# Kernel optimization log

Hardware: AMD Instinct MI355X
Metric: run time of the kernel (lower is better)

Reference implementation:

```python
import jax, jax.numpy as jnp
import numpy as np

B, N, C, H = 8, 1025, 768, 12
HD = C // H  # 64
SCALE = HD ** -0.5


def rotate_half(x):
    x1, x2 = jnp.split(x, 2, axis=-1)
    return jnp.concatenate((-x2, x1), axis=-1)


def apply_rope(x, sin, cos):
    return x * cos + rotate_half(x) * sin


def setup_inputs() -> dict:
    key = jax.random.key(0)
    ks = jax.random.split(key, 7)
    x = jax.random.normal(ks[0], (B, N, C), dtype=jnp.float32)
    sin = jax.random.normal(ks[1], (N - 1, HD), dtype=jnp.float32)
    cos = jax.random.normal(ks[2], (N - 1, HD), dtype=jnp.float32)
    s = 1.0 / np.sqrt(C)
    qkv_w = jax.random.normal(ks[3], (3 * C, C), dtype=jnp.float32) * s
    qkv_b = jnp.zeros((3 * C,), dtype=jnp.float32)
    proj_w = jax.random.normal(ks[4], (C, C), dtype=jnp.float32) * s
    proj_b = jnp.zeros((C,), dtype=jnp.float32)
    return {"x": x, "sin": sin, "cos": cos, "qkv_w": qkv_w, "qkv_b": qkv_b,
            "proj_w": proj_w, "proj_b": proj_b}


def reference(x, sin, cos, qkv_w, qkv_b, proj_w, proj_b):
    b, n, c = x.shape
    qkv = x @ qkv_w.T + qkv_b                      # [B,N,3C]
    qkv = qkv.reshape(b, n, 3, H, HD)
    qkv = jnp.transpose(qkv, (2, 0, 3, 1, 4))      # [3,B,H,N,HD]
    q, k, v = qkv[0], qkv[1], qkv[2]
    # RoPE on patch tokens only (cls token at index 0 excluded)
    q_patch = apply_rope(q[:, :, 1:, :], sin, cos)
    k_patch = apply_rope(k[:, :, 1:, :], sin, cos)
    q = jnp.concatenate((q[:, :, :1, :], q_patch), axis=2)
    k = jnp.concatenate((k[:, :, :1, :], k_patch), axis=2)
    attn = jnp.einsum('bhqd,bhkd->bhqk', q, k) * SCALE
    attn = jax.nn.softmax(attn, axis=-1)
    out = jnp.einsum('bhqk,bhkd->bhqd', attn, v)   # [B,H,N,HD]
    out = jnp.transpose(out, (0, 2, 1, 3)).reshape(b, n, c)
    out = out @ proj_w.T + proj_b
    return out
```

## Files before the change

kernel.cpp:

```cpp
#include <hip/hip_runtime.h>
#include <hip/hip_bf16.h>

constexpr int NTOK   = 1025;
constexpr int M      = 8 * NTOK;
constexpr int MP     = 8448;
constexpr int KDIM   = 768;
constexpr int NQKV   = 2304;
constexpr int NKVPAD = 1088;
constexpr float SCALEL2 = 0.125f * 1.44269504f;

using bf16x8 = __attribute__((ext_vector_type(8))) short;
using f32x4  = __attribute__((ext_vector_type(4))) float;

__device__ __forceinline__ f32x4 mfma_bf16(bf16x8 a, bf16x8 b, f32x4 c) {
  return __builtin_amdgcn_mfma_f32_16x16x32_bf16(a, b, c, 0, 0, 0);
}

__device__ __forceinline__ void gl16(const void* g, void* l) {
  __builtin_amdgcn_global_load_lds(
      (const __attribute__((address_space(1))) void*)g,
      (__attribute__((address_space(3))) void*)l, 16, 0, 0);
}

template <int N> __device__ __forceinline__ void wait_vmcnt() {
  if constexpr (N == 0)
    asm volatile("s_waitcnt vmcnt(0)" ::: "memory");
  else if constexpr (N == 4)
    asm volatile("s_waitcnt vmcnt(4)" ::: "memory");
  else if constexpr (N == 6)
    asm volatile("s_waitcnt vmcnt(6)" ::: "memory");
}

__device__ __forceinline__ float exp2_raw(float x) {
  float r;
  asm("v_exp_f32 %0, %1" : "=v"(r) : "v"(x));
  return r;
}
__device__ __forceinline__ unsigned short cvt_bf16_u16(float x) {
  unsigned u;
  asm("v_cvt_pk_bf16_f32 %0, %1, %2" : "=v"(u) : "v"(x), "v"(x));
  return (unsigned short)(u & 0xffffu);
}
__device__ __forceinline__ __hip_bfloat16 cvt_bf16_raw(float x) {
  union { unsigned short s; __hip_bfloat16 b; } c;
  c.s = cvt_bf16_u16(x);
  return c.b;
}

constexpr size_t SZ_X     = (size_t)MP * KDIM * 2;
constexpr size_t SZ_WQ    = (size_t)NQKV * KDIM * 2;
constexpr size_t SZ_PW    = (size_t)KDIM * KDIM * 2;
constexpr size_t SZ_QK    = (size_t)96 * NTOK * 64 * 2;
constexpr size_t SZ_VT    = (size_t)96 * 64 * NKVPAD * 2;
constexpr size_t OFF_XHI  = 0;
constexpr size_t OFF_WQHI = OFF_XHI + SZ_X;
constexpr size_t OFF_PWHI = OFF_WQHI + SZ_WQ;
constexpr size_t OFF_PWLO = OFF_PWHI + SZ_PW;
constexpr size_t OFF_Q    = OFF_PWLO + SZ_PW;
constexpr size_t OFF_K    = OFF_Q + SZ_QK;
constexpr size_t OFF_VT   = OFF_K + SZ_QK;
constexpr size_t OFF_AO   = OFF_VT + SZ_VT;

constexpr int N4_X  = MP * KDIM / 4;
constexpr int N4_WQ = NQKV * KDIM / 4;
constexpr int N4_PW = KDIM * KDIM / 4;
constexpr int NPADC = NKVPAD - NTOK;
constexpr int N4_PAD = 96 * 64 * NPADC / 4;
constexpr int N4_TOT = N4_X + N4_WQ + N4_PW + N4_PAD;

__global__ void k_prep(const float* __restrict__ x, const float* __restrict__ qkvw,
                       const float* __restrict__ projw,
                       __hip_bfloat16* __restrict__ xhi,
                       __hip_bfloat16* __restrict__ wqhi,
                       __hip_bfloat16* __restrict__ pwhi,
                       __hip_bfloat16* __restrict__ pwlo,
                       __hip_bfloat16* __restrict__ vt) {
  const int u = blockIdx.x * 256 + threadIdx.x;
  if (u < N4_X) {
    const int i = u * 4;
    ushort4 o = {0, 0, 0, 0};
    if (i < M * KDIM) {
      const float4 v = *(const float4*)(x + i);
      o = ushort4{cvt_bf16_u16(v.x), cvt_bf16_u16(v.y), cvt_bf16_u16(v.z),
                  cvt_bf16_u16(v.w)};
    }
    *(ushort4*)((unsigned short*)xhi + i) = o;
  } else if (u < N4_X + N4_WQ) {
    const int i = (u - N4_X) * 4;
    const float4 v = *(const float4*)(qkvw + i);
    *(ushort4*)((unsigned short*)wqhi + i) = ushort4{
        cvt_bf16_u16(v.x), cvt_bf16_u16(v.y), cvt_bf16_u16(v.z), cvt_bf16_u16(v.w)};
  } else if (u < N4_X + N4_WQ + N4_PW) {
    const int i = (u - N4_X - N4_WQ) * 4;
    const float4 v = *(const float4*)(projw + i);
    float vv[4] = {v.x, v.y, v.z, v.w};
    unsigned short h[4], l[4];
#pragma unroll
    for (int k = 0; k < 4; ++k) {
      h[k] = cvt_bf16_u16(vv[k]);
      union { unsigned ui; float f; } c;
      c.ui = (unsigned)h[k] << 16;
      l[k] = cvt_bf16_u16(vv[k] - c.f);
    }
    *(ushort4*)((unsigned short*)pwhi + i) = ushort4{h[0], h[1], h[2], h[3]};
    *(ushort4*)((unsigned short*)pwlo + i) = ushort4{l[0], l[1], l[2], l[3]};
  } else {
    const int e0 = (u - N4_X - N4_WQ - N4_PW) * 4;
#pragma unroll
    for (int k = 0; k < 4; ++k) {
      const int e = e0 + k;
      const int r = e / NPADC;
      const int c = NTOK + (e - r * NPADC);
      vt[(size_t)r * NKVPAD + c] = __float2bfloat16(0.0f);
    }
  }
}

template <int NBX>
__global__ __launch_bounds__(512) void k_gemm_qkv(
    const __hip_bfloat16* __restrict__ A, const __hip_bfloat16* __restrict__ B,
    const float* __restrict__ bias, const float* __restrict__ sinp,
    const float* __restrict__ cosp, __hip_bfloat16* __restrict__ o_q,
    __hip_bfloat16* __restrict__ o_k, __hip_bfloat16* __restrict__ o_vt) {
  const int tid = threadIdx.x;
  const int w = tid >> 6, lane = tid & 63;
  const int wm = w >> 1, wn = w & 1;
  const int l15 = lane & 15, q4 = lane >> 4;

  const int nwg = gridDim.x;
  const int orig = blockIdx.x;
  const int qc = nwg >> 3, rc = nwg & 7;
  const int xcd = orig & 7, o8 = orig >> 3;
  const int wg =
      (xcd < rc ? xcd * (qc + 1) : rc * (qc + 1) + (xcd - rc) * qc) + o8;
  const int bx = wg % NBX, by = wg / NBX;
  const int mBase = by * 256, nBase = bx * 128;

  __shared__ __hip_bfloat16 sm[2][12288];
  constexpr int OFFB = 16384;

  const char* pA = (const char*)A + (size_t)mBase * 1536;
  const char* pB = (const char*)B + (size_t)nBase * 1536;

  int sA_src[2], sA_dst[2], sB_src, sB_dst;
#pragma unroll
  for (int i = 0; i < 2; ++i) {
    const int c = i * 512 + tid;
    const int row = c >> 2;
    sA_src[i] = row * 1536 + (((c & 3) ^ ((row >> 1) & 3)) << 4);
    sA_dst[i] = c << 4;
  }
  {
    const int c = tid;
    const int row = c >> 2;
    sB_src = row * 1536 + (((c & 3) ^ ((row >> 1) & 3)) << 4);
    sB_dst = c << 4;
  }
  auto stage = [&](int kt, int buf) {
    const int kofs = kt * 64;
    char* base = (char*)&sm[buf][0];
#pragma unroll
    for (int i = 0; i < 2; ++i) gl16(pA + sA_src[i] + kofs, base + sA_dst[i]);
    gl16(pB + sB_src + kofs, base + OFFB + sB_dst);
  };

  int fA[4], fB[4];
#pragma unroll
  for (int f = 0; f < 4; ++f) {
    const int ra = wm * 64 + f * 16 + l15;
    const int rb = wn * 64 + f * 16 + l15;
    fA[f] = ra * 64 + ((q4 ^ ((ra >> 1) & 3)) << 4);
    fB[f] = OFFB + rb * 64 + ((q4 ^ ((rb >> 1) & 3)) << 4);
  }

  f32x4 acc[4][4] = {};

  stage(0, 0);
  __syncthreads();

  constexpr int NKT = KDIM / 32;
  for (int kt = 0; kt < NKT; ++kt) {
    const int cur = kt & 1;
    if (kt + 1 < NKT) stage(kt + 1, cur ^ 1);
    const char* s = (const char*)&sm[cur][0];
    bf16x8 a[4], b[4];
#pragma unroll
    for (int f = 0; f < 4; ++f) {
      a[f] = *(const bf16x8*)(s + fA[f]);
      b[f] = *(const bf16x8*)(s + fB[f]);
    }
    __builtin_amdgcn_s_setprio(1);
#pragma unroll
    for (int mt = 0; mt < 4; ++mt)
#pragma unroll
      for (int nt = 0; nt < 4; ++nt)
        acc[mt][nt] = mfma_bf16(a[mt], b[nt], acc[mt][nt]);
    __builtin_amdgcn_s_setprio(0);
    __syncthreads();
  }

#pragma unroll
  for (int mt = 0; mt < 4; ++mt)
#pragma unroll
    for (int j = 0; j < 4; ++j) {
      const int gm = mBase + wm * 64 + mt * 16 + q4 * 4 + j;
      if (gm >= M) continue;
      const int b = gm / NTOK;
      const int t = gm - b * NTOK;
#pragma unroll
      for (int nt = 0; nt < 4; ++nt) {
        const int gc = nBase + wn * 64 + nt * 16 + l15;
        float v = acc[mt][nt][j] + bias[gc];
        const int three = gc / 768;
        const int hd = gc - three * 768;
        const int h = hd >> 6, d = hd & 63;
        const int bh = b * 12 + h;
        if (three == 2) {
          o_vt[((size_t)bh * 64 + d) * NKVPAD + t] = __float2bfloat16(v);
        } else {
          if (t > 0) {
            const float pv = acc[mt][nt ^ 2][j] + bias[gc ^ 32];
            const int so = (t - 1) * 64 + d;
            v = v * cosp[so] + ((d < 32) ? -pv : pv) * sinp[so];
          }
          if (three == 0)
            o_q[((size_t)bh * NTOK + t) * 64 + d] = __float2bfloat16(v);
          else
            o_k[((size_t)bh * NTOK + t) * 64 + d] = __float2bfloat16(v * SCALEL2);
        }
      }
    }
}

template <int NBX>
__global__ __launch_bounds__(256) void k_gemm_proj(
    const __hip_bfloat16* __restrict__ Ahi, const __hip_bfloat16* __restrict__ Asec,
    const __hip_bfloat16* __restrict__ Bhi, const float* __restrict__ bias,
    float* __restrict__ o_f32) {
  const int tid = threadIdx.x;
  const int w = tid >> 6, lane = tid & 63;
  const int wm = w >> 1, wn = w & 1;
  const int l15 = lane & 15, q4 = lane >> 4;

  const int nwg = gridDim.x;
  const int orig = blockIdx.x;
  const int qc = nwg >> 3, rc = nwg & 7;
  const int xcd = orig & 7, o8 = orig >> 3;
  const int wg =
      (xcd < rc ? xcd * (qc + 1) : rc * (qc + 1) + (xcd - rc) * qc) + o8;
  const int bx = wg % NBX, by = wg / NBX;
  const int mBase = by * 128, nBase = bx * 128;

  __shared__ __hip_bfloat16 sm[3][3 * 4096];

  const char* p0 = (const char*)Ahi + (size_t)mBase * (KDIM * 2);
  const char* p1 = (const char*)Asec + (size_t)nBase * (KDIM * 2);
  const char* p2 = (const char*)Bhi + (size_t)nBase * (KDIM * 2);

  const int slog = ((tid & 3) ^ ((tid >> 3) & 3)) << 4;
  const int ph = ((q4 ^ ((l15 >> 1) & 3)) << 4);

  auto stage = [&](int kt, int buf) {
    const int kofs = kt * 64;
    char* base = (char*)sm[buf];
#pragma unroll
    for (int i = 0; i < 2; ++i) {
      const int c = i * 256 + tid;
      const size_t rb = (size_t)(i * 64 + (tid >> 2)) * (KDIM * 2) + slog + kofs;
      gl16(p0 + rb, base + (size_t)c * 16);
      gl16(p1 + rb, base + 8192 + (size_t)c * 16);
      gl16(p2 + rb, base + 16384 + (size_t)c * 16);
    }
  };

  f32x4 acc[4][4] = {};

  stage(0, 0);
  stage(1, 1);

  constexpr int NKT = KDIM / 32;
  for (int kt = 0; kt < NKT; ++kt) {
    if (kt < NKT - 1)
      wait_vmcnt<6>();
    else
      wait_vmcnt<0>();
    __builtin_amdgcn_s_barrier();
    if (kt + 2 < NKT) stage(kt + 2, (kt + 2) % 3);
    char* s0 = (char*)sm[kt % 3];
    char* s1 = s0 + 8192;
    char* s2 = s0 + 16384;
    bf16x8 a0[4], b0[4], b1[4];
#pragma unroll
    for (int mt = 0; mt < 4; ++mt) {
      const int r = wm * 64 + mt * 16 + l15;
      a0[mt] = *(const bf16x8*)(s0 + r * 64 + ph);
    }
#pragma unroll
    for (int nt = 0; nt < 4; ++nt) {
      const int r = wn * 64 + nt * 16 + l15;
      b0[nt] = *(const bf16x8*)(s2 + r * 64 + ph);
      b1[nt] = *(const bf16x8*)(s1 + r * 64 + ph);
    }
    __builtin_amdgcn_s_setprio(1);
#pragma unroll
    for (int mt = 0; mt < 4; ++mt)
#pragma unroll
      for (int nt = 0; nt < 4; ++nt) {
        acc[mt][nt] = mfma_bf16(a0[mt], b0[nt], acc[mt][nt]);
        acc[mt][nt] = mfma_bf16(a0[mt], b1[nt], acc[mt][nt]);
      }
    __builtin_amdgcn_s_setprio(0);
  }

#pragma unroll
  for (int mt = 0; mt < 4; ++mt)
#pragma unroll
    for (int j = 0; j < 4; ++j) {
      const int gm = mBase + wm * 64 + mt * 16 + q4 * 4 + j;
      if (gm >= M) continue;
#pragma unroll
      for (int nt = 0; nt < 4; ++nt) {
        const int gc = nBase + wn * 64 + nt * 16 + l15;
        o_f32[(size_t)gm * 768 + gc] = acc[mt][nt][j] + bias[gc];
      }
    }
}

__global__ __launch_bounds__(256) void k_attn(
    const __hip_bfloat16* __restrict__ Q, const __hip_bfloat16* __restrict__ Kk,
    const __hip_bfloat16* __restrict__ VT, __hip_bfloat16* __restrict__ ao) {
  __shared__ __hip_bfloat16 Kt[3][64 * 64];
  __shared__ __hip_bfloat16 Vt[3][64 * 64];
  __shared__ __hip_bfloat16 Pl[4][32][72];
  const int tid = threadIdx.x, w = tid >> 6, lane = tid & 63;
  const int l15 = lane & 15, q4 = lane >> 4;
  const int id = blockIdx.x;
  const int xcd = id & 7, sub = id >> 3;
  const int hh = sub / 9;
  const int bh = xcd * 12 + hh;
  const int qb = (sub - hh * 9) * 128 + w * 32;
  const size_t qbase = (size_t)bh * NTOK * 64;
  const char* Kb = (const char*)(Kk + qbase);
  const char* Vb = (const char*)(VT + (size_t)bh * 64 * NKVPAD);

  int frag_off[2][4];
#pragma unroll
  for (int f = 0; f < 4; ++f) {
    const int row = f * 16 + l15;
#pragma unroll
    for (int ks = 0; ks < 2; ++ks)
      frag_off[ks][f] = row * 128 + (((ks * 4 + q4) ^ (row & 7)) << 4);
  }
  int stRow[2], sch16[2], stK[2], stV[2], ldsOff[2];
#pragma unroll
  for (int i = 0; i < 2; ++i) {
    const int c = i * 256 + tid;
    const int row = c >> 3;
    stRow[i] = row;
    sch16[i] = ((c & 7) ^ (row & 7)) << 4;
    stK[i] = row * 128 + sch16[i];
    stV[i] = row * (NKVPAD * 2) + sch16[i];
    ldsOff[i] = c * 16;
  }
  int pw_off[2][4], pa_off[2][2];
#pragma unroll
  for (int mt = 0; mt < 2; ++mt) {
#pragma unroll
    for (int j = 0; j < 4; ++j)
      pw_off[mt][j] = ((w * 32 + mt * 16 + q4 * 4 + j) * 72 + l15) * 2;
#pragma unroll
    for (int ks = 0; ks < 2; ++ks)
      pa_off[mt][ks] = ((w * 32 + mt * 16 + l15) * 72 + ks * 32 + q4 * 8) * 2;
  }
  char* Plc = (char*)&Pl[0][0][0];

  bf16x8 qa[2][2];
#pragma unroll
  for (int mt = 0; mt < 2; ++mt) {
    int t = qb + mt * 16 + l15;
    if (t > NTOK - 1) t = NTOK - 1;
#pragma unroll
    for (int ks = 0; ks < 2; ++ks)
      qa[mt][ks] = *(const bf16x8*)(Q + qbase + (size_t)t * 64 + ks * 32 + q4 * 8);
  }

  f32x4 accO[2][4] = {};
  float mrun[2][4], lpart[2][4];
#pragma unroll
  for (int mt = 0; mt < 2; ++mt)
#pragma unroll
    for (int j = 0; j < 4; ++j) {
      mrun[mt][j] = -1e30f;
      lpart[mt][j] = 0.0f;
    }

  auto stageKV = [&](int kt, int b) {
    const int kb0 = kt * 64;
#pragma unroll
    for (int i = 0; i < 2; ++i) {
      const char* srcK;
      if (kt == 16) {
        const int srow = min(kb0 + stRow[i], NTOK - 1);
        srcK = Kb + (size_t)srow * 128 + sch16[i];
      } else {
        srcK = Kb + (size_t)kb0 * 128 + stK[i];
      }
      gl16(srcK, (char*)&Kt[b][0] + ldsOff[i]);
      gl16(Vb + (size_t)kb0 * 2 + stV[i], (char*)&Vt[b][0] + ldsOff[i]);
    }
  };

  auto step = [&](int kt, int cur, bool last) {
    f32x4 s[2][4] = {};
    {
      const char* Kc = (const char*)&Kt[cur][0];
      bf16x8 kfr[2][4];
#pragma unroll
      for (int nt = 0; nt < 4; ++nt)
#pragma unroll
        for (int ks = 0; ks < 2; ++ks)
          kfr[ks][nt] = *(const bf16x8*)(Kc + frag_off[ks][nt]);
      __builtin_amdgcn_s_setprio(1);
#pragma unroll
      for (int mt = 0; mt < 2; ++mt)
#pragma unroll
        for (int nt = 0; nt < 4; ++nt)
#pragma unroll
          for (int ks = 0; ks < 2; ++ks)
            s[mt][nt] = mfma_bf16(qa[mt][ks], kfr[ks][nt], s[mt][nt]);
      __builtin_amdgcn_s_setprio(0);
    }
    if (last) {
#pragma unroll
      for (int nt = 0; nt < 4; ++nt)
        if (1024 + nt * 16 + l15 > NTOK - 1) {
#pragma unroll
          for (int mt = 0; mt < 2; ++mt)
#pragma unroll
            for (int j = 0; j < 4; ++j) s[mt][nt][j] = -1e30f;
        }
    }
    float smax[2][4];
    bool okl = true;
#pragma unroll
    for (int mt = 0; mt < 2; ++mt)
#pragma unroll
      for (int j = 0; j < 4; ++j) {
        const float a =
            fmaxf(fmaxf(s[mt][0][j], s[mt][1][j]), fmaxf(s[mt][2][j], s[mt][3][j]));
        smax[mt][j] = a;
        okl = okl && (a <= mrun[mt][j] + 8.0f);
      }
    if (!__all((int)okl)) {
#pragma unroll
      for (int mt = 0; mt < 2; ++mt)
#pragma unroll
        for (int j = 0; j < 4; ++j) {
          float m0 = smax[mt][j];
#pragma unroll
          for (int off = 1; off < 16; off <<= 1) m0 = fmaxf(m0, __shfl_xor(m0, off));
          const float mnew = fmaxf(mrun[mt][j], m0);
          const float fsc = exp2_raw(mrun[mt][j] - mnew);
          lpart[mt][j] *= fsc;
          mrun[mt][j] = mnew;
#pragma unroll
          for (int nd = 0; nd < 4; ++nd) accO[mt][nd][j] *= fsc;
        }
    }
#pragma unroll
    for (int mt = 0; mt < 2; ++mt)
#pragma unroll
      for (int j = 0; j < 4; ++j) {
        float acc = 0.0f;
        char* pw = Plc + pw_off[mt][j];
#pragma unroll
        for (int nt = 0; nt < 4; ++nt) {
          const float p = exp2_raw(s[mt][nt][j] - mrun[mt][j]);
          acc += p;
          *(__hip_bfloat16*)(pw + nt * 32) = cvt_bf16_raw(p);
        }
        lpart[mt][j] += acc;
      }
    bf16x8 pa[2][2], vf[2][4];
#pragma unroll
    for (int mt = 0; mt < 2; ++mt)
#pragma unroll
      for (int ks = 0; ks < 2; ++ks)
        pa[mt][ks] = *(const bf16x8*)(Plc + pa_off[mt][ks]);
    {
      const char* Vc = (const char*)&Vt[cur][0];
#pragma unroll
      for (int nd = 0; nd < 4; ++nd)
#pragma unroll
        for (int ks = 0; ks < 2; ++ks)
          vf[ks][nd] = *(const bf16x8*)(Vc + frag_off[ks][nd]);
    }
    __builtin_amdgcn_s_setprio(1);
#pragma unroll
    for (int mt = 0; mt < 2; ++mt)
#pragma unroll
      for (int nd = 0; nd < 4; ++nd)
#pragma unroll
        for (int ks = 0; ks < 2; ++ks)
          accO[mt][nd] = mfma_bf16(pa[mt][ks], vf[ks][nd], accO[mt][nd]);
    __builtin_amdgcn_s_setprio(0);
  };

  stageKV(0, 0);
  stageKV(1, 1);
  for (int kt = 0; kt < 17; ++kt) {
    if (kt < 16)
      wait_vmcnt<4>();
    else
      wait_vmcnt<0>();
    __builtin_amdgcn_s_barrier();
    if (kt + 2 < 17) stageKV(kt + 2, (kt + 2) % 3);
    step(kt, kt % 3, kt == 16);
  }

  const int b = bh / 12, h = bh - (bh / 12) * 12;
#pragma unroll
  for (int mt = 0; mt < 2; ++mt)
#pragma unroll
    for (int j = 0; j < 4; ++j) {
      float sum = lpart[mt][j];
#pragma unroll
      for (int off2 = 1; off2 < 16; off2 <<= 1) sum += __shfl_xor(sum, off2);
      const int t = qb + mt * 16 + q4 * 4 + j;
      if (t > NTOK - 1) continue;
      const float inv = 1.0f / sum;
      const size_t ro = ((size_t)(b * NTOK + t)) * 768 + h * 64;
#pragma unroll
      for (int nd = 0; nd < 4; ++nd) {
        const int d = nd * 16 + l15;
        ao[ro + d] = __float2bfloat16(accO[mt][nd][j] * inv);
      }
    }
}

extern "C" void kernel_launch(void* const* d_in, const int* in_sizes, int n_in,
                              void* d_out, int out_size, void* d_ws, size_t ws_size,
                              hipStream_t stream) {
  const float* x = (const float*)d_in[0];
  const float* sinp = (const float*)d_in[1];
  const float* cosp = (const float*)d_in[2];
  const float* qkvw = (const float*)d_in[3];
  const float* qkvb = (const float*)d_in[4];
  const float* projw = (const float*)d_in[5];
  const float* projb = (const float*)d_in[6];

  char* ws = (char*)d_ws;
  __hip_bfloat16* xhi = (__hip_bfloat16*)(ws + OFF_XHI);
  __hip_bfloat16* wqhi = (__hip_bfloat16*)(ws + OFF_WQHI);
  __hip_bfloat16* pwhi = (__hip_bfloat16*)(ws + OFF_PWHI);
  __hip_bfloat16* pwlo = (__hip_bfloat16*)(ws + OFF_PWLO);
  __hip_bfloat16* qb = (__hip_bfloat16*)(ws + OFF_Q);
  __hip_bfloat16* kb = (__hip_bfloat16*)(ws + OFF_K);
  __hip_bfloat16* vt = (__hip_bfloat16*)(ws + OFF_VT);
  __hip_bfloat16* ao = (__hip_bfloat16*)(ws + OFF_AO);

  k_prep<<<N4_TOT / 256, 256, 0, stream>>>(x, qkvw, projw, xhi, wqhi, pwhi, pwlo,
                                           vt);
  k_gemm_qkv<18><<<dim3(18 * 33), 512, 0, stream>>>(xhi, wqhi, qkvb, sinp, cosp,
                                                    qb, kb, vt);
  k_attn<<<dim3(864), 256, 0, stream>>>(qb, kb, vt, ao);
  k_gemm_proj<6><<<dim3(6 * 66), 256, 0, stream>>>(ao, pwlo, pwhi, projb,
                                                   (float*)d_out);
}
```

Before: 235.6 us.

## Retile QKV GEMM to 128x256 with 4 waves and triple-buffered LDS pipeline

The QKV projection GEMM moves from 256x128 tiles with 8 waves to 128x256 tiles with 4 waves, each wave computing a 64x128 sub-tile. LDS staging changes from double to triple buffering, using vmcnt waits and a raw barrier in place of __syncthreads, so global loads run two k-steps ahead. The padded M shrinks to 8320, which reduces the number of M tiles for both GEMMs. The aim is more MFMA work per LDS read and better overlap of loads with compute, at the cost of higher register pressure from 32 accumulators per wave and more LDS per block.

```diff
diff --git a/kernel.cpp b/kernel.cpp
--- a/kernel.cpp
+++ b/kernel.cpp
@@ -3,7 +3,7 @@
 
 constexpr int NTOK   = 1025;
 constexpr int M      = 8 * NTOK;
-constexpr int MP     = 8448;
+constexpr int MP     = 8320;
 constexpr int KDIM   = 768;
 constexpr int NQKV   = 2304;
 constexpr int NKVPAD = 1088;
@@ -117,7 +117,7 @@
 }
 
 template <int NBX>
-__global__ __launch_bounds__(512) void k_gemm_qkv(
+__global__ __launch_bounds__(256) void k_gemm_qkv(
     const __hip_bfloat16* __restrict__ A, const __hip_bfloat16* __restrict__ B,
     const float* __restrict__ bias, const float* __restrict__ sinp,
     const float* __restrict__ cosp, __hip_bfloat16* __restrict__ o_q,
@@ -134,69 +134,76 @@
   const int wg =
       (xcd < rc ? xcd * (qc + 1) : rc * (qc + 1) + (xcd - rc) * qc) + o8;
   const int bx = wg % NBX, by = wg / NBX;
-  const int mBase = by * 256, nBase = bx * 128;
-
-  __shared__ __hip_bfloat16 sm[2][12288];
-  constexpr int OFFB = 16384;
+  const int mBase = by * 128, nBase = bx * 256;
+
+  __shared__ __hip_bfloat16 sm[3][12288];
+  constexpr int OFFB = 8192;
 
   const char* pA = (const char*)A + (size_t)mBase * 1536;
   const char* pB = (const char*)B + (size_t)nBase * 1536;
 
-  int sA_src[2], sA_dst[2], sB_src, sB_dst;
+  int sA_src[2], sA_dst[2], sB_src[4], sB_dst[4];
 #pragma unroll
   for (int i = 0; i < 2; ++i) {
-    const int c = i * 512 + tid;
+    const int c = i * 256 + tid;
     const int row = c >> 2;
     sA_src[i] = row * 1536 + (((c & 3) ^ ((row >> 1) & 3)) << 4);
     sA_dst[i] = c << 4;
   }
-  {
-    const int c = tid;
+#pragma unroll
+  for (int i = 0; i < 4; ++i) {
+    const int c = i * 256 + tid;
     const int row = c >> 2;
-    sB_src = row * 1536 + (((c & 3) ^ ((row >> 1) & 3)) << 4);
-    sB_dst = c << 4;
+    sB_src[i] = row * 1536 + (((c & 3) ^ ((row >> 1) & 3)) << 4);
+    sB_dst[i] = OFFB + (c << 4);
   }
   auto stage = [&](int kt, int buf) {
     const int kofs = kt * 64;
     char* base = (char*)&sm[buf][0];
 #pragma unroll
     for (int i = 0; i < 2; ++i) gl16(pA + sA_src[i] + kofs, base + sA_dst[i]);
-    gl16(pB + sB_src + kofs, base + OFFB + sB_dst);
+#pragma unroll
+    for (int i = 0; i < 4; ++i) gl16(pB + sB_src[i] + kofs, base + sB_dst[i]);
   };
 
-  int fA[4], fB[4];
+  int fA[4], fB[8];
 #pragma unroll
   for (int f = 0; f < 4; ++f) {
     const int ra = wm * 64 + f * 16 + l15;
-    const int rb = wn * 64 + f * 16 + l15;
     fA[f] = ra * 64 + ((q4 ^ ((ra >> 1) & 3)) << 4);
+  }
+#pragma unroll
+  for (int f = 0; f < 8; ++f) {
+    const int rb = wn * 128 + f * 16 + l15;
     fB[f] = OFFB + rb * 64 + ((q4 ^ ((rb >> 1) & 3)) << 4);
   }
 
-  f32x4 acc[4][4] = {};
+  f32x4 acc[4][8] = {};
 
   stage(0, 0);
-  __syncthreads();
+  stage(1, 1);
 
   constexpr int NKT = KDIM / 32;
   for (int kt = 0; kt < NKT; ++kt) {
-    const int cur = kt & 1;
-    if (kt + 1 < NKT) stage(kt + 1, cur ^ 1);
-    const char* s = (const char*)&sm[cur][0];
-    bf16x8 a[4], b[4];
-#pragma unroll
-    for (int f = 0; f < 4; ++f) {
-      a[f] = *(const bf16x8*)(s + fA[f]);
-      b[f] = *(const bf16x8*)(s + fB[f]);
-    }
+    if (kt < NKT - 1)
+      wait_vmcnt<6>();
+    else
+      wait_vmcnt<0>();
+    __builtin_amdgcn_s_barrier();
+    if (kt + 2 < NKT) stage(kt + 2, (kt + 2) % 3);
+    const char* s = (const char*)&sm[kt % 3][0];
+    bf16x8 a[4], b[8];
+#pragma unroll
+    for (int f = 0; f < 4; ++f) a[f] = *(const bf16x8*)(s + fA[f]);
+#pragma unroll
+    for (int f = 0; f < 8; ++f) b[f] = *(const bf16x8*)(s + fB[f]);
     __builtin_amdgcn_s_setprio(1);
 #pragma unroll
     for (int mt = 0; mt < 4; ++mt)
 #pragma unroll
-      for (int nt = 0; nt < 4; ++nt)
+      for (int nt = 0; nt < 8; ++nt)
         acc[mt][nt] = mfma_bf16(a[mt], b[nt], acc[mt][nt]);
     __builtin_amdgcn_s_setprio(0);
-    __syncthreads();
   }
 
 #pragma unroll
@@ -208,8 +215,8 @@
       const int b = gm / NTOK;
       const int t = gm - b * NTOK;
 #pragma unroll
-      for (int nt = 0; nt < 4; ++nt) {
-        const int gc = nBase + wn * 64 + nt * 16 + l15;
+      for (int nt = 0; nt < 8; ++nt) {
+        const int gc = nBase + wn * 128 + nt * 16 + l15;
         float v = acc[mt][nt][j] + bias[gc];
         const int three = gc / 768;
         const int hd = gc - three * 768;
@@ -561,9 +568,9 @@
 
   k_prep<<<N4_TOT / 256, 256, 0, stream>>>(x, qkvw, projw, xhi, wqhi, pwhi, pwlo,
                                            vt);
-  k_gemm_qkv<18><<<dim3(18 * 33), 512, 0, stream>>>(xhi, wqhi, qkvb, sinp, cosp,
-                                                    qb, kb, vt);
+  k_gemm_qkv<9><<<dim3(9 * 65), 256, 0, stream>>>(xhi, wqhi, qkvb, sinp, cosp,
+                                                  qb, kb, vt);
   k_attn<<<dim3(864), 256, 0, stream>>>(qb, kb, vt, ao);
-  k_gemm_proj<6><<<dim3(6 * 66), 256, 0, stream>>>(ao, pwlo, pwhi, projb,
+  k_gemm_proj<6><<<dim3(6 * 65), 256, 0, stream>>>(ao, pwlo, pwhi, projb,
                                                    (float*)d_out);
 }
```

Result: slower. 293.7 us (+24.7%).

## Drop proj weight low split and enlarge QKV GEMM tile with triple buffering

Applied to the files above, without the earlier changes.

The projection GEMM no longer uses the hi/lo bf16 split of the weights. It now runs a single bf16 MFMA per tile, which halves its MFMA work and LDS traffic, and the prep kernel stops writing the low part. The QKV GEMM grows its tile from 256x128 to 256x256, with 8 waves arranged 2x4 and each wave covering a 128x64 slab. It also moves from a double-buffered __syncthreads pipeline to a three-stage global_load_lds pipeline using vmcnt waits. The larger tile and 48KB of LDS per buffer set give more reuse but fewer workgroups (297) and more accumulator registers, and dropping the low split reduces projection precision.

```diff
diff --git a/kernel.cpp b/kernel.cpp
--- a/kernel.cpp
+++ b/kernel.cpp
@@ -55,8 +55,7 @@
 constexpr size_t OFF_XHI  = 0;
 constexpr size_t OFF_WQHI = OFF_XHI + SZ_X;
 constexpr size_t OFF_PWHI = OFF_WQHI + SZ_WQ;
-constexpr size_t OFF_PWLO = OFF_PWHI + SZ_PW;
-constexpr size_t OFF_Q    = OFF_PWLO + SZ_PW;
+constexpr size_t OFF_Q    = OFF_PWHI + SZ_PW;
 constexpr size_t OFF_K    = OFF_Q + SZ_QK;
 constexpr size_t OFF_VT   = OFF_K + SZ_QK;
 constexpr size_t OFF_AO   = OFF_VT + SZ_VT;
@@ -73,7 +72,6 @@
                        __hip_bfloat16* __restrict__ xhi,
                        __hip_bfloat16* __restrict__ wqhi,
                        __hip_bfloat16* __restrict__ pwhi,
-                       __hip_bfloat16* __restrict__ pwlo,
                        __hip_bfloat16* __restrict__ vt) {
   const int u = blockIdx.x * 256 + threadIdx.x;
   if (u < N4_X) {
@@ -93,17 +91,8 @@
   } else if (u < N4_X + N4_WQ + N4_PW) {
     const int i = (u - N4_X - N4_WQ) * 4;
     const float4 v = *(const float4*)(projw + i);
-    float vv[4] = {v.x, v.y, v.z, v.w};
-    unsigned short h[4], l[4];
-#pragma unroll
-    for (int k = 0; k < 4; ++k) {
-      h[k] = cvt_bf16_u16(vv[k]);
-      union { unsigned ui; float f; } c;
-      c.ui = (unsigned)h[k] << 16;
-      l[k] = cvt_bf16_u16(vv[k] - c.f);
-    }
-    *(ushort4*)((unsigned short*)pwhi + i) = ushort4{h[0], h[1], h[2], h[3]};
-    *(ushort4*)((unsigned short*)pwlo + i) = ushort4{l[0], l[1], l[2], l[3]};
+    *(ushort4*)((unsigned short*)pwhi + i) = ushort4{
+        cvt_bf16_u16(v.x), cvt_bf16_u16(v.y), cvt_bf16_u16(v.z), cvt_bf16_u16(v.w)};
   } else {
     const int e0 = (u - N4_X - N4_WQ - N4_PW) * 4;
 #pragma unroll
@@ -124,7 +113,7 @@
     __hip_bfloat16* __restrict__ o_k, __hip_bfloat16* __restrict__ o_vt) {
   const int tid = threadIdx.x;
   const int w = tid >> 6, lane = tid & 63;
-  const int wm = w >> 1, wn = w & 1;
+  const int wm = w >> 2, wn = w & 3;
   const int l15 = lane & 15, q4 = lane >> 4;
 
   const int nwg = gridDim.x;
@@ -134,76 +123,77 @@
   const int wg =
       (xcd < rc ? xcd * (qc + 1) : rc * (qc + 1) + (xcd - rc) * qc) + o8;
   const int bx = wg % NBX, by = wg / NBX;
-  const int mBase = by * 256, nBase = bx * 128;
-
-  __shared__ __hip_bfloat16 sm[2][12288];
+  const int mBase = by * 256, nBase = bx * 256;
+
+  __shared__ __hip_bfloat16 sm[3][16384];
   constexpr int OFFB = 16384;
 
   const char* pA = (const char*)A + (size_t)mBase * 1536;
   const char* pB = (const char*)B + (size_t)nBase * 1536;
 
-  int sA_src[2], sA_dst[2], sB_src, sB_dst;
+  int sSrc[2], sDst[2];
 #pragma unroll
   for (int i = 0; i < 2; ++i) {
     const int c = i * 512 + tid;
     const int row = c >> 2;
-    sA_src[i] = row * 1536 + (((c & 3) ^ ((row >> 1) & 3)) << 4);
-    sA_dst[i] = c << 4;
-  }
-  {
-    const int c = tid;
-    const int row = c >> 2;
-    sB_src = row * 1536 + (((c & 3) ^ ((row >> 1) & 3)) << 4);
-    sB_dst = c << 4;
+    sSrc[i] = row * 1536 + (((c & 3) ^ ((row >> 1) & 3)) << 4);
+    sDst[i] = c << 4;
   }
   auto stage = [&](int kt, int buf) {
     const int kofs = kt * 64;
     char* base = (char*)&sm[buf][0];
 #pragma unroll
-    for (int i = 0; i < 2; ++i) gl16(pA + sA_src[i] + kofs, base + sA_dst[i]);
-    gl16(pB + sB_src + kofs, base + OFFB + sB_dst);
+    for (int i = 0; i < 2; ++i) {
+      gl16(pA + sSrc[i] + kofs, base + sDst[i]);
+      gl16(pB + sSrc[i] + kofs, base + OFFB + sDst[i]);
+    }
   };
 
-  int fA[4], fB[4];
+  int fA[8], fB[4];
+#pragma unroll
+  for (int f = 0; f < 8; ++f) {
+    const int ra = wm * 128 + f * 16 + l15;
+    fA[f] = ra * 64 + ((q4 ^ ((ra >> 1) & 3)) << 4);
+  }
 #pragma unroll
   for (int f = 0; f < 4; ++f) {
-    const int ra = wm * 64 + f * 16 + l15;
     const int rb = wn * 64 + f * 16 + l15;
-    fA[f] = ra * 64 + ((q4 ^ ((ra >> 1) & 3)) << 4);
     fB[f] = OFFB + rb * 64 + ((q4 ^ ((rb >> 1) & 3)) << 4);
   }
 
-  f32x4 acc[4][4] = {};
+  f32x4 acc[8][4] = {};
 
   stage(0, 0);
-  __syncthreads();
+  stage(1, 1);
 
   constexpr int NKT = KDIM / 32;
   for (int kt = 0; kt < NKT; ++kt) {
-    const int cur = kt & 1;
-    if (kt + 1 < NKT) stage(kt + 1, cur ^ 1);
-    const char* s = (const char*)&sm[cur][0];
-    bf16x8 a[4], b[4];
-#pragma unroll
-    for (int f = 0; f < 4; ++f) {
-      a[f] = *(const bf16x8*)(s + fA[f]);
-      b[f] = *(const bf16x8*)(s + fB[f]);
-    }
+    if (kt < NKT - 1)
+      wait_vmcnt<4>();
+    else
+      wait_vmcnt<0>();
+    __builtin_amdgcn_s_barrier();
+    if (kt + 2 < NKT) stage(kt + 2, (kt + 2) % 3);
+    const char* s = (const char*)&sm[kt % 3][0];
+    bf16x8 a[8], b[4];
+#pragma unroll
+    for (int f = 0; f < 8; ++f) a[f] = *(const bf16x8*)(s + fA[f]);
+#pragma unroll
+    for (int f = 0; f < 4; ++f) b[f] = *(const bf16x8*)(s + fB[f]);
     __builtin_amdgcn_s_setprio(1);
 #pragma unroll
-    for (int mt = 0; mt < 4; ++mt)
+    for (int mt = 0; mt < 8; ++mt)
 #pragma unroll
       for (int nt = 0; nt < 4; ++nt)
         acc[mt][nt] = mfma_bf16(a[mt], b[nt], acc[mt][nt]);
     __builtin_amdgcn_s_setprio(0);
-    __syncthreads();
-  }
-
-#pragma unroll
-  for (int mt = 0; mt < 4; ++mt)
+  }
+
+#pragma unroll
+  for (int mt = 0; mt < 8; ++mt)
 #pragma unroll
     for (int j = 0; j < 4; ++j) {
-      const int gm = mBase + wm * 64 + mt * 16 + q4 * 4 + j;
+      const int gm = mBase + wm * 128 + mt * 16 + q4 * 4 + j;
       if (gm >= M) continue;
       const int b = gm / NTOK;
       const int t = gm - b * NTOK;
@@ -234,9 +224,8 @@
 
 template <int NBX>
 __global__ __launch_bounds__(256) void k_gemm_proj(
-    const __hip_bfloat16* __restrict__ Ahi, const __hip_bfloat16* __restrict__ Asec,
-    const __hip_bfloat16* __restrict__ Bhi, const float* __restrict__ bias,
-    float* __restrict__ o_f32) {
+    const __hip_bfloat16* __restrict__ Ain, const __hip_bfloat16* __restrict__ Bhi,
+    const float* __restrict__ bias, float* __restrict__ o_f32) {
   const int tid = threadIdx.x;
   const int w = tid >> 6, lane = tid & 63;
   const int wm = w >> 1, wn = w & 1;
@@ -251,10 +240,10 @@
   const int bx = wg % NBX, by = wg / NBX;
   const int mBase = by * 128, nBase = bx * 128;
 
-  __shared__ __hip_bfloat16 sm[3][3 * 4096];
-
-  const char* p0 = (const char*)Ahi + (size_t)mBase * (KDIM * 2);
-  const char* p1 = (const char*)Asec + (size_t)nBase * (KDIM * 2);
+  __shared__ __hip_bfloat16 sm[3][2 * 4096];
+  constexpr int OFFB = 8192;
+
+  const char* p0 = (const char*)Ain + (size_t)mBase * (KDIM * 2);
   const char* p2 = (const char*)Bhi + (size_t)nBase * (KDIM * 2);
 
   const int slog = ((tid & 3) ^ ((tid >> 3) & 3)) << 4;
@@ -268,8 +257,7 @@
       const int c = i * 256 + tid;
       const size_t rb = (size_t)(i * 64 + (tid >> 2)) * (KDIM * 2) + slog + kofs;
       gl16(p0 + rb, base + (size_t)c * 16);
-      gl16(p1 + rb, base + 8192 + (size_t)c * 16);
-      gl16(p2 + rb, base + 16384 + (size_t)c * 16);
+      gl16(p2 + rb, base + OFFB + (size_t)c * 16);
     }
   };
 
@@ -281,15 +269,14 @@
   constexpr int NKT = KDIM / 32;
   for (int kt = 0; kt < NKT; ++kt) {
     if (kt < NKT - 1)
-      wait_vmcnt<6>();
+      wait_vmcnt<4>();
     else
       wait_vmcnt<0>();
     __builtin_amdgcn_s_barrier();
     if (kt + 2 < NKT) stage(kt + 2, (kt + 2) % 3);
     char* s0 = (char*)sm[kt % 3];
-    char* s1 = s0 + 8192;
-    char* s2 = s0 + 16384;
-    bf16x8 a0[4], b0[4], b1[4];
+    char* s2 = s0 + OFFB;
+    bf16x8 a0[4], b0[4];
 #pragma unroll
     for (int mt = 0; mt < 4; ++mt) {
       const int r = wm * 64 + mt * 16 + l15;
@@ -299,16 +286,13 @@
     for (int nt = 0; nt < 4; ++nt) {
       const int r = wn * 64 + nt * 16 + l15;
       b0[nt] = *(const bf16x8*)(s2 + r * 64 + ph);
-      b1[nt] = *(const bf16x8*)(s1 + r * 64 + ph);
     }
     __builtin_amdgcn_s_setprio(1);
 #pragma unroll
     for (int mt = 0; mt < 4; ++mt)
 #pragma unroll
-      for (int nt = 0; nt < 4; ++nt) {
+      for (int nt = 0; nt < 4; ++nt)
         acc[mt][nt] = mfma_bf16(a0[mt], b0[nt], acc[mt][nt]);
-        acc[mt][nt] = mfma_bf16(a0[mt], b1[nt], acc[mt][nt]);
-      }
     __builtin_amdgcn_s_setprio(0);
   }
 
@@ -553,17 +537,15 @@
   __hip_bfloat16* xhi = (__hip_bfloat16*)(ws + OFF_XHI);
   __hip_bfloat16* wqhi = (__hip_bfloat16*)(ws + OFF_WQHI);
   __hip_bfloat16* pwhi = (__hip_bfloat16*)(ws + OFF_PWHI);
-  __hip_bfloat16* pwlo = (__hip_bfloat16*)(ws + OFF_PWLO);
   __hip_bfloat16* qb = (__hip_bfloat16*)(ws + OFF_Q);
   __hip_bfloat16* kb = (__hip_bfloat16*)(ws + OFF_K);
   __hip_bfloat16* vt = (__hip_bfloat16*)(ws + OFF_VT);
   __hip_bfloat16* ao = (__hip_bfloat16*)(ws + OFF_AO);
 
-  k_prep<<<N4_TOT / 256, 256, 0, stream>>>(x, qkvw, projw, xhi, wqhi, pwhi, pwlo,
-                                           vt);
-  k_gemm_qkv<18><<<dim3(18 * 33), 512, 0, stream>>>(xhi, wqhi, qkvb, sinp, cosp,
-                                                    qb, kb, vt);
+  k_prep<<<N4_TOT / 256, 256, 0, stream>>>(x, qkvw, projw, xhi, wqhi, pwhi, vt);
+  k_gemm_qkv<9><<<dim3(9 * 33), 512, 0, stream>>>(xhi, wqhi, qkvb, sinp, cosp,
+                                                  qb, kb, vt);
   k_attn<<<dim3(864), 256, 0, stream>>>(qb, kb, vt, ao);
-  k_gemm_proj<6><<<dim3(6 * 66), 256, 0, stream>>>(ao, pwlo, pwhi, projb,
+  k_gemm_proj<6><<<dim3(6 * 66), 256, 0, stream>>>(ao, pwhi, projb,
                                                    (float*)d_out);
 }
```

Result: slower. 243.4 us (+3.3%).
